# Performance work log

Measured on AMD Instinct MI355X. Metric: run time of the kernel, lower is better.

Reference implementation:

```python
import jax, jax.numpy as jnp
import numpy as np

# Tsit5 (Tsitouras 2011) explicit RK tableau coefficients (5th-order solution weights)
A21 = 0.161
A31, A32 = -0.008480655492356989, 0.335480655492357
A41, A42, A43 = 2.8971530571054935, -6.359448489975075, 4.3622954328695815
A51, A52, A53, A54 = 5.325864828439257, -11.748883564062828, 7.4955393428898365, -0.09249506636175525
A61, A62, A63, A64, A65 = 5.86145544294642, -12.92096931784711, 8.159367898576159, -0.071584973281401, -0.028269050394068383
B1, B2, B3, B4, B5, B6 = 0.09646076681806523, 0.01, 0.4798896504144996, 1.379008574103742, -3.290069515436081, 2.324710524099774

BATCH, D, H, T = 4096, 64, 256, 128


def net_apply(y, W1, b1, W2, b2):
    # y: [B, D] -> dy/dt: [B, D]  (MLP vector field, autonomous)
    return jnp.tanh(y @ W1 + b1) @ W2 + b2


def tsit5_step(f, y, h):
    # One explicit Tsit5 step of size h on state y: [B, D]
    k1 = f(y)
    k2 = f(y + h * (A21 * k1))
    k3 = f(y + h * (A31 * k1 + A32 * k2))
    k4 = f(y + h * (A41 * k1 + A42 * k2 + A43 * k3))
    k5 = f(y + h * (A51 * k1 + A52 * k2 + A53 * k3 + A54 * k4))
    k6 = f(y + h * (A61 * k1 + A62 * k2 + A63 * k3 + A64 * k4 + A65 * k5))
    return y + h * (B1 * k1 + B2 * k2 + B3 * k3 + B4 * k4 + B5 * k5 + B6 * k6)


def setup_inputs() -> dict:
    key = jax.random.key(0)
    k0, k1, k2 = jax.random.split(key, 3)
    y0 = jax.random.normal(k0, (BATCH, D), dtype=jnp.float32)
    ts = jnp.arange(T, dtype=jnp.float32) * 0.05  # save times
    W1 = jax.random.normal(k1, (D, H), dtype=jnp.float32) / np.sqrt(D)
    b1 = jnp.zeros((H,), dtype=jnp.float32)
    W2 = jax.random.normal(k2, (H, D), dtype=jnp.float32) / np.sqrt(H)
    b2 = jnp.zeros((D,), dtype=jnp.float32)
    return {"y0": y0, "ts": ts, "W1": W1, "b1": b1, "W2": W2, "b2": b2, "n_sub": 8}


def reference(y0, ts, W1, b1, W2, b2, n_sub):
    # Integrate dy/dt = net(y) with fixed-step Tsit5 (n_sub substeps per save interval),
    # returning the trajectory at save points ts: [B, T, D].
    f = lambda y: net_apply(y, W1, b1, W2, b2)

    def interval(y, dt):
        h = dt / n_sub
        def sub(yc, _):
            return tsit5_step(f, yc, h), None
        y, _ = jax.lax.scan(sub, y, None, length=n_sub)
        return y, y

    dts = jnp.diff(ts)                      # [T-1]
    _, ys = jax.lax.scan(interval, y0, dts)  # [T-1, B, D]
    traj = jnp.concatenate([y0[None], ys], axis=0)  # [T, B, D]
    return jnp.transpose(traj, (1, 0, 2))   # [B, T, D]
```

## Files before the change

### kernel.cpp

```cpp
#include <hip/hip_runtime.h>
#include <hip/hip_bf16.h>

typedef __bf16 bf16x8 __attribute__((ext_vector_type(8)));
typedef float f32x4 __attribute__((ext_vector_type(4)));

#define MFMA_B16(a,b,c) __builtin_amdgcn_mfma_f32_16x16x32_bf16((a),(b),(c),0,0,0)

#define A21f 0.161f
#define A31f (-0.008480655492356989f)
#define A32f 0.335480655492357f
#define A41f 2.8971530571054935f
#define A42f (-6.359448489975075f)
#define A43f 4.3622954328695815f
#define A51f 5.325864828439257f
#define A52f (-11.748883564062828f)
#define A53f 7.4955393428898365f
#define A54f (-0.09249506636175525f)
#define A61f 5.86145544294642f
#define A62f (-12.92096931784711f)
#define A63f 8.159367898576159f
#define A64f (-0.071584973281401f)
#define A65f (-0.028269050394068383f)
#define B1f 0.09646076681806523f
#define B2f 0.01f
#define B3f 0.4798896504144996f
#define B4f 1.379008574103742f
#define B5f (-3.290069515436081f)
#define B6f 2.324710524099774f

constexpr int T_SAVE = 128;
constexpr int DIM = 64;
constexpr int HID = 256;

__device__ __forceinline__ float fast_exp2(float x){
#if __has_builtin(__builtin_amdgcn_exp2f)
  return __builtin_amdgcn_exp2f(x);
#else
  return exp2f(x);
#endif
}
__device__ __forceinline__ float fast_rcp(float x){
#if __has_builtin(__builtin_amdgcn_rcpf)
  return __builtin_amdgcn_rcpf(x);
#else
  return 1.0f / x;
#endif
}
__device__ __forceinline__ float tanh_fast(float x){
  float t = fast_exp2(x * 2.8853900817779268f);
  return 1.0f - 2.0f * fast_rcp(t + 1.0f);
}

__global__ __launch_bounds__(512, 2)
void node_tsit5_kernel(const float* __restrict__ y0, const float* __restrict__ ts,
                       const float* __restrict__ W1g, const float* __restrict__ b1g,
                       const float* __restrict__ W2g, const float* __restrict__ b2g,
                       const int* __restrict__ nsub_p, float* __restrict__ out)
{
  const int tid = (int)threadIdx.x;
  const int w   = tid >> 6;
  const int l   = tid & 63;
  const int c   = l & 15;
  const int g   = l >> 4;
  const int wq  = w & 3;
  const int kh  = w >> 2;
  const bool hiW = (kh == 0);
  const int rowbase = (int)blockIdx.x * 16;

  __shared__ __align__(16) __bf16 Yh[2*64*8];
  __shared__ __align__(16) __bf16 Yl[2*64*8];
  __shared__ __align__(16) __bf16 Hh[8*64*8];
  __shared__ __align__(16) __bf16 Hl[8*64*8];
  __shared__ __align__(16) f32x4 Pex[8*64];
  __shared__ float ts_s[T_SAVE];

  if (tid < T_SAVE) ts_s[tid] = ts[tid];

  const int nsub = nsub_p[0];

  bf16x8 w1h[2][2], w1l[2][2], w2h[4], w2l[4];
#pragma unroll
  for (int nt = 0; nt < 2; ++nt) {
    const int col = (2*w + nt)*16 + c;
#pragma unroll
    for (int ks = 0; ks < 2; ++ks)
#pragma unroll
      for (int j = 0; j < 8; ++j) {
        float v = W1g[(ks*32 + g*8 + j)*HID + col];
        __bf16 hi = (__bf16)v;
        w1h[nt][ks][j] = hi;
        w1l[nt][ks][j] = (__bf16)(v - (float)hi);
      }
  }
#pragma unroll
  for (int i = 0; i < 4; ++i) {
    const int ks = 4*kh + i;
#pragma unroll
    for (int j = 0; j < 8; ++j) {
      float v = W2g[(ks*32 + g*8 + j)*DIM + (wq*16 + c)];
      __bf16 hi = (__bf16)v;
      w2h[i][j] = hi;
      w2l[i][j] = (__bf16)(v - (float)hi);
    }
  }
  float b1v[2];
#pragma unroll
  for (int nt = 0; nt < 2; ++nt) b1v[nt] = b1g[(2*w + nt)*16 + c];
  const float b2v = b2g[wq*16 + c];

  const int d_    = wq*16 + c;
  const int physL = l ^ ((l >> 3) & 3);

  int yoff[4];
#pragma unroll
  for (int s = 0; s < 4; ++s) {
    int row = 4*g + s;
    int lp  = row | (((d_ >> 3) & 3) << 4);
    int ph  = lp ^ ((lp >> 3) & 3);
    yoff[s] = (d_ >> 5)*512 + ph*8 + (d_ & 7);
  }
  int hoff[2][4];
#pragma unroll
  for (int nt = 0; nt < 2; ++nt) {
    int jcol = (2*w + nt)*16 + c;
#pragma unroll
    for (int r = 0; r < 4; ++r) {
      int row = 4*g + r;
      int lp  = row | (((jcol >> 3) & 3) << 4);
      int ph  = lp ^ ((lp >> 3) & 3);
      hoff[nt][r] = (jcol >> 5)*512 + ph*8 + (jcol & 7);
    }
  }

  float y[4];
#pragma unroll
  for (int s = 0; s < 4; ++s) {
    int row = rowbase + 4*g + s;
    y[s] = y0[row*DIM + d_];
    if (hiW) out[(size_t)row*(T_SAVE*DIM) + d_] = y[s];
  }
  __syncthreads();

  float k1[4], k2[4], k3[4], k4[4], k5[4], k6[4], ysv[4];
#pragma unroll
  for (int s = 0; s < 4; ++s) ysv[s] = y[s];

  auto feval = [&](float (&kout)[4]) {
#pragma unroll
    for (int s = 0; s < 4; ++s) {
      __bf16 hi = (__bf16)ysv[s];
      if (hiW) Yh[yoff[s]] = hi;
      else     Yl[yoff[s]] = (__bf16)(ysv[s] - (float)hi);
    }
    __syncthreads();
    bf16x8 ah0 = *(const bf16x8*)&Yh[physL*8];
    bf16x8 ah1 = *(const bf16x8*)&Yh[512 + physL*8];
    bf16x8 al0 = *(const bf16x8*)&Yl[physL*8];
    bf16x8 al1 = *(const bf16x8*)&Yl[512 + physL*8];
    f32x4 acc[2];
#pragma unroll
    for (int nt = 0; nt < 2; ++nt) acc[nt] = f32x4{0.f,0.f,0.f,0.f};
#pragma unroll
    for (int nt = 0; nt < 2; ++nt) acc[nt] = MFMA_B16(ah0, w1h[nt][0], acc[nt]);
#pragma unroll
    for (int nt = 0; nt < 2; ++nt) acc[nt] = MFMA_B16(ah1, w1h[nt][1], acc[nt]);
#pragma unroll
    for (int nt = 0; nt < 2; ++nt) acc[nt] = MFMA_B16(ah0, w1l[nt][0], acc[nt]);
#pragma unroll
    for (int nt = 0; nt < 2; ++nt) acc[nt] = MFMA_B16(ah1, w1l[nt][1], acc[nt]);
#pragma unroll
    for (int nt = 0; nt < 2; ++nt) acc[nt] = MFMA_B16(al0, w1h[nt][0], acc[nt]);
#pragma unroll
    for (int nt = 0; nt < 2; ++nt) acc[nt] = MFMA_B16(al1, w1h[nt][1], acc[nt]);
#pragma unroll
    for (int nt = 0; nt < 2; ++nt)
#pragma unroll
      for (int r = 0; r < 4; ++r) {
        float th = tanh_fast(acc[nt][r] + b1v[nt]);
        __bf16 hi = (__bf16)th;
        Hh[hoff[nt][r]] = hi;
        Hl[hoff[nt][r]] = (__bf16)(th - (float)hi);
      }
    __syncthreads();
    f32x4 a2[3];
#pragma unroll
    for (int i = 0; i < 3; ++i) a2[i] = f32x4{0.f,0.f,0.f,0.f};
#pragma unroll
    for (int i = 0; i < 4; ++i) {
      const int ks = 4*kh + i;
      bf16x8 ah = *(const bf16x8*)&Hh[ks*512 + physL*8];
      bf16x8 al = *(const bf16x8*)&Hl[ks*512 + physL*8];
      a2[0] = MFMA_B16(ah, w2h[i], a2[0]);
      a2[1] = MFMA_B16(ah, w2l[i], a2[1]);
      a2[2] = MFMA_B16(al, w2h[i], a2[2]);
    }
    f32x4 ps = (a2[0] + a2[1]) + a2[2];
    Pex[w*64 + l] = ps;
    __syncthreads();
    f32x4 qs = Pex[(w ^ 4)*64 + l];
#pragma unroll
    for (int s = 0; s < 4; ++s)
      kout[s] = (ps[s] + qs[s]) + b2v;
  };

  for (int iv = 0; iv < T_SAVE-1; ++iv) {
    const float h = (ts_s[iv+1] - ts_s[iv]) / (float)nsub;
    for (int sub = 0; sub < nsub; ++sub) {
      feval(k1);
#pragma unroll
      for (int s = 0; s < 4; ++s) ysv[s] = fmaf(h, A21f*k1[s], y[s]);
      feval(k2);
#pragma unroll
      for (int s = 0; s < 4; ++s) {
        float t = fmaf(A32f, k2[s], A31f*k1[s]);
        ysv[s] = fmaf(h, t, y[s]);
      }
      feval(k3);
#pragma unroll
      for (int s = 0; s < 4; ++s) {
        float t = A41f*k1[s];
        t = fmaf(A42f, k2[s], t);
        t = fmaf(A43f, k3[s], t);
        ysv[s] = fmaf(h, t, y[s]);
      }
      feval(k4);
#pragma unroll
      for (int s = 0; s < 4; ++s) {
        float t = A51f*k1[s];
        t = fmaf(A52f, k2[s], t);
        t = fmaf(A53f, k3[s], t);
        t = fmaf(A54f, k4[s], t);
        ysv[s] = fmaf(h, t, y[s]);
      }
      feval(k5);
#pragma unroll
      for (int s = 0; s < 4; ++s) {
        float t = A61f*k1[s];
        t = fmaf(A62f, k2[s], t);
        t = fmaf(A63f, k3[s], t);
        t = fmaf(A64f, k4[s], t);
        t = fmaf(A65f, k5[s], t);
        ysv[s] = fmaf(h, t, y[s]);
      }
      feval(k6);
#pragma unroll
      for (int s = 0; s < 4; ++s) {
        float t = B1f*k1[s];
        t = fmaf(B2f, k2[s], t);
        t = fmaf(B3f, k3[s], t);
        t = fmaf(B4f, k4[s], t);
        t = fmaf(B5f, k5[s], t);
        t = fmaf(B6f, k6[s], t);
        y[s] = fmaf(h, t, y[s]);
        ysv[s] = y[s];
      }
    }
    if (hiW) {
#pragma unroll
      for (int s = 0; s < 4; ++s) {
        int row = rowbase + 4*g + s;
        out[(size_t)row*(T_SAVE*DIM) + (size_t)(iv+1)*DIM + d_] = y[s];
      }
    }
  }
}

extern "C" void kernel_launch(void* const* d_in, const int* in_sizes, int n_in,
                              void* d_out, int out_size, void* d_ws, size_t ws_size,
                              hipStream_t stream) {
  const float* y0 = (const float*)d_in[0];
  const float* ts = (const float*)d_in[1];
  const float* W1 = (const float*)d_in[2];
  const float* b1 = (const float*)d_in[3];
  const float* W2 = (const float*)d_in[4];
  const float* b2 = (const float*)d_in[5];
  const int* nsub = (const int*)d_in[6];
  float* out = (float*)d_out;

  const int Bnum = in_sizes[0] / DIM;
  const int nblocks = Bnum / 16;
  node_tsit5_kernel<<<nblocks, 512, 0, stream>>>(y0, ts, W1, b1, W2, b2, nsub, out);
}
```

Measured before the change: 7.033 ms.

## Split per-block work across 16 waves with four-way K reduction

Doubles the block to 1024 threads (16 waves), so each wave computes one 16-column hidden tile and a quarter of the second-layer K range instead of two tiles and half. The partial sums of the second layer are reduced four ways through shared memory, and only the first 8 waves hold the RK state. This is meant to shorten the per-wave serial MFMA chain in each function evaluation by spreading it over more waves. In exchange it adds more threads waiting at every barrier, a larger reduction buffer, and 8 waves that sit idle during the RK stage updates.

```diff
diff --git a/kernel.cpp b/kernel.cpp
--- a/kernel.cpp
+++ b/kernel.cpp
@@ -51,7 +51,7 @@
   return 1.0f - 2.0f * fast_rcp(t + 1.0f);
 }
 
-__global__ __launch_bounds__(512, 2)
+__global__ __launch_bounds__(1024, 4)
 void node_tsit5_kernel(const float* __restrict__ y0, const float* __restrict__ ts,
                        const float* __restrict__ W1g, const float* __restrict__ b1g,
                        const float* __restrict__ W2g, const float* __restrict__ b2g,
@@ -63,38 +63,35 @@
   const int c   = l & 15;
   const int g   = l >> 4;
   const int wq  = w & 3;
-  const int kh  = w >> 2;
-  const bool hiW = (kh == 0);
+  const int kq  = w >> 2;
+  const bool stateW = (kq < 2);
+  const bool hiW    = (kq == 0);
   const int rowbase = (int)blockIdx.x * 16;
 
   __shared__ __align__(16) __bf16 Yh[2*64*8];
   __shared__ __align__(16) __bf16 Yl[2*64*8];
   __shared__ __align__(16) __bf16 Hh[8*64*8];
   __shared__ __align__(16) __bf16 Hl[8*64*8];
-  __shared__ __align__(16) f32x4 Pex[8*64];
+  __shared__ __align__(16) f32x4 Pex[16*64];
   __shared__ float ts_s[T_SAVE];
 
   if (tid < T_SAVE) ts_s[tid] = ts[tid];
 
   const int nsub = nsub_p[0];
 
-  bf16x8 w1h[2][2], w1l[2][2], w2h[4], w2l[4];
-#pragma unroll
-  for (int nt = 0; nt < 2; ++nt) {
-    const int col = (2*w + nt)*16 + c;
-#pragma unroll
-    for (int ks = 0; ks < 2; ++ks)
-#pragma unroll
-      for (int j = 0; j < 8; ++j) {
-        float v = W1g[(ks*32 + g*8 + j)*HID + col];
-        __bf16 hi = (__bf16)v;
-        w1h[nt][ks][j] = hi;
-        w1l[nt][ks][j] = (__bf16)(v - (float)hi);
-      }
-  }
-#pragma unroll
-  for (int i = 0; i < 4; ++i) {
-    const int ks = 4*kh + i;
+  bf16x8 w1h[2], w1l[2], w2h[2], w2l[2];
+#pragma unroll
+  for (int ks = 0; ks < 2; ++ks)
+#pragma unroll
+    for (int j = 0; j < 8; ++j) {
+      float v = W1g[(ks*32 + g*8 + j)*HID + (w*16 + c)];
+      __bf16 hi = (__bf16)v;
+      w1h[ks][j] = hi;
+      w1l[ks][j] = (__bf16)(v - (float)hi);
+    }
+#pragma unroll
+  for (int i = 0; i < 2; ++i) {
+    const int ks = 2*kq + i;
 #pragma unroll
     for (int j = 0; j < 8; ++j) {
       float v = W2g[(ks*32 + g*8 + j)*DIM + (wq*16 + c)];
@@ -103,9 +100,7 @@
       w2l[i][j] = (__bf16)(v - (float)hi);
     }
   }
-  float b1v[2];
-#pragma unroll
-  for (int nt = 0; nt < 2; ++nt) b1v[nt] = b1g[(2*w + nt)*16 + c];
+  const float b1v = b1g[w*16 + c];
   const float b2v = b2g[wq*16 + c];
 
   const int d_    = wq*16 + c;
@@ -119,25 +114,26 @@
     int ph  = lp ^ ((lp >> 3) & 3);
     yoff[s] = (d_ >> 5)*512 + ph*8 + (d_ & 7);
   }
-  int hoff[2][4];
-#pragma unroll
-  for (int nt = 0; nt < 2; ++nt) {
-    int jcol = (2*w + nt)*16 + c;
+  int hoff[4];
+  {
+    int jcol = w*16 + c;
 #pragma unroll
     for (int r = 0; r < 4; ++r) {
       int row = 4*g + r;
       int lp  = row | (((jcol >> 3) & 3) << 4);
       int ph  = lp ^ ((lp >> 3) & 3);
-      hoff[nt][r] = (jcol >> 5)*512 + ph*8 + (jcol & 7);
-    }
-  }
-
-  float y[4];
-#pragma unroll
-  for (int s = 0; s < 4; ++s) {
-    int row = rowbase + 4*g + s;
-    y[s] = y0[row*DIM + d_];
-    if (hiW) out[(size_t)row*(T_SAVE*DIM) + d_] = y[s];
+      hoff[r] = (jcol >> 5)*512 + ph*8 + (jcol & 7);
+    }
+  }
+
+  float y[4] = {0.f,0.f,0.f,0.f};
+  if (stateW) {
+#pragma unroll
+    for (int s = 0; s < 4; ++s) {
+      int row = rowbase + 4*g + s;
+      y[s] = y0[row*DIM + d_];
+      if (hiW) out[(size_t)row*(T_SAVE*DIM) + d_] = y[s];
+    }
   }
   __syncthreads();
 
@@ -146,113 +142,120 @@
   for (int s = 0; s < 4; ++s) ysv[s] = y[s];
 
   auto feval = [&](float (&kout)[4]) {
-#pragma unroll
-    for (int s = 0; s < 4; ++s) {
-      __bf16 hi = (__bf16)ysv[s];
-      if (hiW) Yh[yoff[s]] = hi;
-      else     Yl[yoff[s]] = (__bf16)(ysv[s] - (float)hi);
+    if (stateW) {
+#pragma unroll
+      for (int s = 0; s < 4; ++s) {
+        __bf16 hi = (__bf16)ysv[s];
+        if (hiW) Yh[yoff[s]] = hi;
+        else     Yl[yoff[s]] = (__bf16)(ysv[s] - (float)hi);
+      }
     }
     __syncthreads();
     bf16x8 ah0 = *(const bf16x8*)&Yh[physL*8];
     bf16x8 ah1 = *(const bf16x8*)&Yh[512 + physL*8];
     bf16x8 al0 = *(const bf16x8*)&Yl[physL*8];
     bf16x8 al1 = *(const bf16x8*)&Yl[512 + physL*8];
-    f32x4 acc[2];
-#pragma unroll
-    for (int nt = 0; nt < 2; ++nt) acc[nt] = f32x4{0.f,0.f,0.f,0.f};
-#pragma unroll
-    for (int nt = 0; nt < 2; ++nt) acc[nt] = MFMA_B16(ah0, w1h[nt][0], acc[nt]);
-#pragma unroll
-    for (int nt = 0; nt < 2; ++nt) acc[nt] = MFMA_B16(ah1, w1h[nt][1], acc[nt]);
-#pragma unroll
-    for (int nt = 0; nt < 2; ++nt) acc[nt] = MFMA_B16(ah0, w1l[nt][0], acc[nt]);
-#pragma unroll
-    for (int nt = 0; nt < 2; ++nt) acc[nt] = MFMA_B16(ah1, w1l[nt][1], acc[nt]);
-#pragma unroll
-    for (int nt = 0; nt < 2; ++nt) acc[nt] = MFMA_B16(al0, w1h[nt][0], acc[nt]);
-#pragma unroll
-    for (int nt = 0; nt < 2; ++nt) acc[nt] = MFMA_B16(al1, w1h[nt][1], acc[nt]);
-#pragma unroll
-    for (int nt = 0; nt < 2; ++nt)
-#pragma unroll
-      for (int r = 0; r < 4; ++r) {
-        float th = tanh_fast(acc[nt][r] + b1v[nt]);
-        __bf16 hi = (__bf16)th;
-        Hh[hoff[nt][r]] = hi;
-        Hl[hoff[nt][r]] = (__bf16)(th - (float)hi);
-      }
+    f32x4 acc0 = {0.f,0.f,0.f,0.f}, acc1 = {0.f,0.f,0.f,0.f};
+    acc0 = MFMA_B16(ah0, w1h[0], acc0);
+    acc1 = MFMA_B16(ah1, w1h[1], acc1);
+    acc0 = MFMA_B16(ah0, w1l[0], acc0);
+    acc1 = MFMA_B16(ah1, w1l[1], acc1);
+    acc0 = MFMA_B16(al0, w1h[0], acc0);
+    acc1 = MFMA_B16(al1, w1h[1], acc1);
+    f32x4 hsum = acc0 + acc1;
+#pragma unroll
+    for (int r = 0; r < 4; ++r) {
+      float th = tanh_fast(hsum[r] + b1v);
+      __bf16 hi = (__bf16)th;
+      Hh[hoff[r]] = hi;
+      Hl[hoff[r]] = (__bf16)(th - (float)hi);
+    }
     __syncthreads();
-    f32x4 a2[3];
-#pragma unroll
-    for (int i = 0; i < 3; ++i) a2[i] = f32x4{0.f,0.f,0.f,0.f};
-#pragma unroll
-    for (int i = 0; i < 4; ++i) {
-      const int ks = 4*kh + i;
+    f32x4 aA = {0.f,0.f,0.f,0.f}, aB = {0.f,0.f,0.f,0.f};
+#pragma unroll
+    for (int i = 0; i < 2; ++i) {
+      const int ks = 2*kq + i;
       bf16x8 ah = *(const bf16x8*)&Hh[ks*512 + physL*8];
       bf16x8 al = *(const bf16x8*)&Hl[ks*512 + physL*8];
-      a2[0] = MFMA_B16(ah, w2h[i], a2[0]);
-      a2[1] = MFMA_B16(ah, w2l[i], a2[1]);
-      a2[2] = MFMA_B16(al, w2h[i], a2[2]);
-    }
-    f32x4 ps = (a2[0] + a2[1]) + a2[2];
-    Pex[w*64 + l] = ps;
+      aA = MFMA_B16(ah, w2h[i], aA);
+      aB = MFMA_B16(ah, w2l[i], aB);
+      aB = MFMA_B16(al, w2h[i], aB);
+    }
+    Pex[w*64 + l] = aA + aB;
     __syncthreads();
-    f32x4 qs = Pex[(w ^ 4)*64 + l];
-#pragma unroll
-    for (int s = 0; s < 4; ++s)
-      kout[s] = (ps[s] + qs[s]) + b2v;
+    if (stateW) {
+      f32x4 q0 = Pex[(wq     )*64 + l];
+      f32x4 q1 = Pex[(wq +  4)*64 + l];
+      f32x4 q2 = Pex[(wq +  8)*64 + l];
+      f32x4 q3 = Pex[(wq + 12)*64 + l];
+      f32x4 kk = (q0 + q1) + (q2 + q3);
+#pragma unroll
+      for (int s = 0; s < 4; ++s) kout[s] = kk[s] + b2v;
+    }
   };
 
   for (int iv = 0; iv < T_SAVE-1; ++iv) {
     const float h = (ts_s[iv+1] - ts_s[iv]) / (float)nsub;
     for (int sub = 0; sub < nsub; ++sub) {
       feval(k1);
-#pragma unroll
-      for (int s = 0; s < 4; ++s) ysv[s] = fmaf(h, A21f*k1[s], y[s]);
+      if (stateW) {
+#pragma unroll
+        for (int s = 0; s < 4; ++s) ysv[s] = fmaf(h, A21f*k1[s], y[s]);
+      }
       feval(k2);
-#pragma unroll
-      for (int s = 0; s < 4; ++s) {
-        float t = fmaf(A32f, k2[s], A31f*k1[s]);
-        ysv[s] = fmaf(h, t, y[s]);
+      if (stateW) {
+#pragma unroll
+        for (int s = 0; s < 4; ++s) {
+          float t = fmaf(A32f, k2[s], A31f*k1[s]);
+          ysv[s] = fmaf(h, t, y[s]);
+        }
       }
       feval(k3);
-#pragma unroll
-      for (int s = 0; s < 4; ++s) {
-        float t = A41f*k1[s];
-        t = fmaf(A42f, k2[s], t);
-        t = fmaf(A43f, k3[s], t);
-        ysv[s] = fmaf(h, t, y[s]);
+      if (stateW) {
+#pragma unroll
+        for (int s = 0; s < 4; ++s) {
+          float t = A41f*k1[s];
+          t = fmaf(A42f, k2[s], t);
+          t = fmaf(A43f, k3[s], t);
+          ysv[s] = fmaf(h, t, y[s]);
+        }
       }
       feval(k4);
-#pragma unroll
-      for (int s = 0; s < 4; ++s) {
-        float t = A51f*k1[s];
-        t = fmaf(A52f, k2[s], t);
-        t = fmaf(A53f, k3[s], t);
-        t = fmaf(A54f, k4[s], t);
-        ysv[s] = fmaf(h, t, y[s]);
+      if (stateW) {
+#pragma unroll
+        for (int s = 0; s < 4; ++s) {
+          float t = A51f*k1[s];
+          t = fmaf(A52f, k2[s], t);
+          t = fmaf(A53f, k3[s], t);
+          t = fmaf(A54f, k4[s], t);
+          ysv[s] = fmaf(h, t, y[s]);
+        }
       }
       feval(k5);
-#pragma unroll
-      for (int s = 0; s < 4; ++s) {
-        float t = A61f*k1[s];
-        t = fmaf(A62f, k2[s], t);
-        t = fmaf(A63f, k3[s], t);
-        t = fmaf(A64f, k4[s], t);
-        t = fmaf(A65f, k5[s], t);
-        ysv[s] = fmaf(h, t, y[s]);
+      if (stateW) {
+#pragma unroll
+        for (int s = 0; s < 4; ++s) {
+          float t = A61f*k1[s];
+          t = fmaf(A62f, k2[s], t);
+          t = fmaf(A63f, k3[s], t);
+          t = fmaf(A64f, k4[s], t);
+          t = fmaf(A65f, k5[s], t);
+          ysv[s] = fmaf(h, t, y[s]);
+        }
       }
       feval(k6);
-#pragma unroll
-      for (int s = 0; s < 4; ++s) {
-        float t = B1f*k1[s];
-        t = fmaf(B2f, k2[s], t);
-        t = fmaf(B3f, k3[s], t);
-        t = fmaf(B4f, k4[s], t);
-        t = fmaf(B5f, k5[s], t);
-        t = fmaf(B6f, k6[s], t);
-        y[s] = fmaf(h, t, y[s]);
-        ysv[s] = y[s];
+      if (stateW) {
+#pragma unroll
+        for (int s = 0; s < 4; ++s) {
+          float t = B1f*k1[s];
+          t = fmaf(B2f, k2[s], t);
+          t = fmaf(B3f, k3[s], t);
+          t = fmaf(B4f, k4[s], t);
+          t = fmaf(B5f, k5[s], t);
+          t = fmaf(B6f, k6[s], t);
+          y[s] = fmaf(h, t, y[s]);
+          ysv[s] = y[s];
+        }
       }
     }
     if (hiW) {
@@ -279,5 +282,5 @@
 
   const int Bnum = in_sizes[0] / DIM;
   const int nblocks = Bnum / 16;
-  node_tsit5_kernel<<<nblocks, 512, 0, stream>>>(y0, ts, W1, b1, W2, b2, nsub, out);
-}
+  node_tsit5_kernel<<<nblocks, 1024, 0, stream>>>(y0, ts, W1, b1, W2, b2, nsub, out);
+}
```

New measurement: 7.325 ms. 4.1% more time.

## Drop cross-wave partial-sum exchange by giving each wave the full W2 K-range

Applied to the files above, without the earlier changes.

Each wave now holds all eight K-slices of W2 in registers and computes the full second-layer product, so the shared-memory partial-sum exchange and its extra barrier per function evaluation are removed. The first-layer MFMAs are split into two independent accumulator chains to shorten dependency stalls, and the RK stage combinations are expressed as 4-wide vector arithmetic. The trade-off is that every wave does twice the second-layer MFMA work, pairs of waves compute the same output redundantly, and register pressure rises, which may hurt occupancy under the 512x2 launch bound.

```diff
diff --git a/kernel.cpp b/kernel.cpp
--- a/kernel.cpp
+++ b/kernel.cpp
@@ -50,6 +50,7 @@
   float t = fast_exp2(x * 2.8853900817779268f);
   return 1.0f - 2.0f * fast_rcp(t + 1.0f);
 }
+__device__ __forceinline__ f32x4 splat4(float x){ return f32x4{x,x,x,x}; }
 
 __global__ __launch_bounds__(512, 2)
 void node_tsit5_kernel(const float* __restrict__ y0, const float* __restrict__ ts,
@@ -63,22 +64,20 @@
   const int c   = l & 15;
   const int g   = l >> 4;
   const int wq  = w & 3;
-  const int kh  = w >> 2;
-  const bool hiW = (kh == 0);
+  const bool hiW = (w < 4);
   const int rowbase = (int)blockIdx.x * 16;
 
   __shared__ __align__(16) __bf16 Yh[2*64*8];
   __shared__ __align__(16) __bf16 Yl[2*64*8];
   __shared__ __align__(16) __bf16 Hh[8*64*8];
   __shared__ __align__(16) __bf16 Hl[8*64*8];
-  __shared__ __align__(16) f32x4 Pex[8*64];
   __shared__ float ts_s[T_SAVE];
 
   if (tid < T_SAVE) ts_s[tid] = ts[tid];
 
   const int nsub = nsub_p[0];
 
-  bf16x8 w1h[2][2], w1l[2][2], w2h[4], w2l[4];
+  bf16x8 w1h[2][2], w1l[2][2];
 #pragma unroll
   for (int nt = 0; nt < 2; ++nt) {
     const int col = (2*w + nt)*16 + c;
@@ -92,17 +91,16 @@
         w1l[nt][ks][j] = (__bf16)(v - (float)hi);
       }
   }
-#pragma unroll
-  for (int i = 0; i < 4; ++i) {
-    const int ks = 4*kh + i;
+  bf16x8 w2h[8], w2l[8];
+#pragma unroll
+  for (int ks = 0; ks < 8; ++ks)
 #pragma unroll
     for (int j = 0; j < 8; ++j) {
       float v = W2g[(ks*32 + g*8 + j)*DIM + (wq*16 + c)];
       __bf16 hi = (__bf16)v;
-      w2h[i][j] = hi;
-      w2l[i][j] = (__bf16)(v - (float)hi);
-    }
-  }
+      w2h[ks][j] = hi;
+      w2l[ks][j] = (__bf16)(v - (float)hi);
+    }
   float b1v[2];
 #pragma unroll
   for (int nt = 0; nt < 2; ++nt) b1v[nt] = b1g[(2*w + nt)*16 + c];
@@ -132,134 +130,110 @@
     }
   }
 
-  float y[4];
+  f32x4 y4;
 #pragma unroll
   for (int s = 0; s < 4; ++s) {
     int row = rowbase + 4*g + s;
-    y[s] = y0[row*DIM + d_];
-    if (hiW) out[(size_t)row*(T_SAVE*DIM) + d_] = y[s];
+    y4[s] = y0[row*DIM + d_];
+    if (hiW) out[(size_t)row*(T_SAVE*DIM) + d_] = y4[s];
   }
   __syncthreads();
 
-  float k1[4], k2[4], k3[4], k4[4], k5[4], k6[4], ysv[4];
-#pragma unroll
-  for (int s = 0; s < 4; ++s) ysv[s] = y[s];
-
-  auto feval = [&](float (&kout)[4]) {
-#pragma unroll
-    for (int s = 0; s < 4; ++s) {
-      __bf16 hi = (__bf16)ysv[s];
-      if (hiW) Yh[yoff[s]] = hi;
-      else     Yl[yoff[s]] = (__bf16)(ysv[s] - (float)hi);
+  f32x4 ysv = y4;
+
+  auto feval = [&]() -> f32x4 {
+    if (hiW) {
+#pragma unroll
+      for (int s = 0; s < 4; ++s) Yh[yoff[s]] = (__bf16)ysv[s];
+    } else {
+#pragma unroll
+      for (int s = 0; s < 4; ++s) {
+        float hi = (float)(__bf16)ysv[s];
+        Yl[yoff[s]] = (__bf16)(ysv[s] - hi);
+      }
     }
     __syncthreads();
     bf16x8 ah0 = *(const bf16x8*)&Yh[physL*8];
     bf16x8 ah1 = *(const bf16x8*)&Yh[512 + physL*8];
     bf16x8 al0 = *(const bf16x8*)&Yl[physL*8];
     bf16x8 al1 = *(const bf16x8*)&Yl[512 + physL*8];
-    f32x4 acc[2];
-#pragma unroll
-    for (int nt = 0; nt < 2; ++nt) acc[nt] = f32x4{0.f,0.f,0.f,0.f};
-#pragma unroll
-    for (int nt = 0; nt < 2; ++nt) acc[nt] = MFMA_B16(ah0, w1h[nt][0], acc[nt]);
-#pragma unroll
-    for (int nt = 0; nt < 2; ++nt) acc[nt] = MFMA_B16(ah1, w1h[nt][1], acc[nt]);
-#pragma unroll
-    for (int nt = 0; nt < 2; ++nt) acc[nt] = MFMA_B16(ah0, w1l[nt][0], acc[nt]);
-#pragma unroll
-    for (int nt = 0; nt < 2; ++nt) acc[nt] = MFMA_B16(ah1, w1l[nt][1], acc[nt]);
-#pragma unroll
-    for (int nt = 0; nt < 2; ++nt) acc[nt] = MFMA_B16(al0, w1h[nt][0], acc[nt]);
-#pragma unroll
-    for (int nt = 0; nt < 2; ++nt) acc[nt] = MFMA_B16(al1, w1h[nt][1], acc[nt]);
-#pragma unroll
-    for (int nt = 0; nt < 2; ++nt)
-#pragma unroll
-      for (int r = 0; r < 4; ++r) {
-        float th = tanh_fast(acc[nt][r] + b1v[nt]);
-        __bf16 hi = (__bf16)th;
-        Hh[hoff[nt][r]] = hi;
-        Hl[hoff[nt][r]] = (__bf16)(th - (float)hi);
-      }
+    f32x4 p0 = {0.f,0.f,0.f,0.f}, q0 = {0.f,0.f,0.f,0.f};
+    f32x4 p1 = {0.f,0.f,0.f,0.f}, q1 = {0.f,0.f,0.f,0.f};
+    p0 = MFMA_B16(ah0, w1h[0][0], p0);  q0 = MFMA_B16(ah1, w1h[0][1], q0);
+    p1 = MFMA_B16(ah0, w1h[1][0], p1);  q1 = MFMA_B16(ah1, w1h[1][1], q1);
+    p0 = MFMA_B16(ah0, w1l[0][0], p0);  q0 = MFMA_B16(ah1, w1l[0][1], q0);
+    p1 = MFMA_B16(ah0, w1l[1][0], p1);  q1 = MFMA_B16(ah1, w1l[1][1], q1);
+    p0 = MFMA_B16(al0, w1h[0][0], p0);  q0 = MFMA_B16(al1, w1h[0][1], q0);
+    p1 = MFMA_B16(al0, w1h[1][0], p1);  q1 = MFMA_B16(al1, w1h[1][1], q1);
+    f32x4 h0 = p0 + q0, h1 = p1 + q1;
+#pragma unroll
+    for (int r = 0; r < 4; ++r) {
+      float th = tanh_fast(h0[r] + b1v[0]);
+      __bf16 hi = (__bf16)th;
+      Hh[hoff[0][r]] = hi;
+      Hl[hoff[0][r]] = (__bf16)(th - (float)hi);
+    }
+#pragma unroll
+    for (int r = 0; r < 4; ++r) {
+      float th = tanh_fast(h1[r] + b1v[1]);
+      __bf16 hi = (__bf16)th;
+      Hh[hoff[1][r]] = hi;
+      Hl[hoff[1][r]] = (__bf16)(th - (float)hi);
+    }
     __syncthreads();
-    f32x4 a2[3];
-#pragma unroll
-    for (int i = 0; i < 3; ++i) a2[i] = f32x4{0.f,0.f,0.f,0.f};
-#pragma unroll
-    for (int i = 0; i < 4; ++i) {
-      const int ks = 4*kh + i;
+    f32x4 aA = {0.f,0.f,0.f,0.f}, aB = {0.f,0.f,0.f,0.f}, aC = {0.f,0.f,0.f,0.f};
+#pragma unroll
+    for (int ks = 0; ks < 8; ++ks) {
       bf16x8 ah = *(const bf16x8*)&Hh[ks*512 + physL*8];
       bf16x8 al = *(const bf16x8*)&Hl[ks*512 + physL*8];
-      a2[0] = MFMA_B16(ah, w2h[i], a2[0]);
-      a2[1] = MFMA_B16(ah, w2l[i], a2[1]);
-      a2[2] = MFMA_B16(al, w2h[i], a2[2]);
-    }
-    f32x4 ps = (a2[0] + a2[1]) + a2[2];
-    Pex[w*64 + l] = ps;
-    __syncthreads();
-    f32x4 qs = Pex[(w ^ 4)*64 + l];
-#pragma unroll
-    for (int s = 0; s < 4; ++s)
-      kout[s] = (ps[s] + qs[s]) + b2v;
+      aA = MFMA_B16(ah, w2h[ks], aA);
+      aB = MFMA_B16(ah, w2l[ks], aB);
+      aC = MFMA_B16(al, w2h[ks], aC);
+    }
+    return (aA + aB) + aC + splat4(b2v);
   };
 
   for (int iv = 0; iv < T_SAVE-1; ++iv) {
     const float h = (ts_s[iv+1] - ts_s[iv]) / (float)nsub;
+    const f32x4 h4 = splat4(h);
     for (int sub = 0; sub < nsub; ++sub) {
-      feval(k1);
-#pragma unroll
-      for (int s = 0; s < 4; ++s) ysv[s] = fmaf(h, A21f*k1[s], y[s]);
-      feval(k2);
-#pragma unroll
-      for (int s = 0; s < 4; ++s) {
-        float t = fmaf(A32f, k2[s], A31f*k1[s]);
-        ysv[s] = fmaf(h, t, y[s]);
-      }
-      feval(k3);
-#pragma unroll
-      for (int s = 0; s < 4; ++s) {
-        float t = A41f*k1[s];
-        t = fmaf(A42f, k2[s], t);
-        t = fmaf(A43f, k3[s], t);
-        ysv[s] = fmaf(h, t, y[s]);
-      }
-      feval(k4);
-#pragma unroll
-      for (int s = 0; s < 4; ++s) {
-        float t = A51f*k1[s];
-        t = fmaf(A52f, k2[s], t);
-        t = fmaf(A53f, k3[s], t);
-        t = fmaf(A54f, k4[s], t);
-        ysv[s] = fmaf(h, t, y[s]);
-      }
-      feval(k5);
-#pragma unroll
-      for (int s = 0; s < 4; ++s) {
-        float t = A61f*k1[s];
-        t = fmaf(A62f, k2[s], t);
-        t = fmaf(A63f, k3[s], t);
-        t = fmaf(A64f, k4[s], t);
-        t = fmaf(A65f, k5[s], t);
-        ysv[s] = fmaf(h, t, y[s]);
-      }
-      feval(k6);
-#pragma unroll
-      for (int s = 0; s < 4; ++s) {
-        float t = B1f*k1[s];
-        t = fmaf(B2f, k2[s], t);
-        t = fmaf(B3f, k3[s], t);
-        t = fmaf(B4f, k4[s], t);
-        t = fmaf(B5f, k5[s], t);
-        t = fmaf(B6f, k6[s], t);
-        y[s] = fmaf(h, t, y[s]);
-        ysv[s] = y[s];
+      f32x4 k1 = feval();
+      ysv = y4 + h4 * (splat4(A21f) * k1);
+      f32x4 k2 = feval();
+      {
+        f32x4 t = splat4(A31f)*k1 + splat4(A32f)*k2;
+        ysv = y4 + h4 * t;
+      }
+      f32x4 k3 = feval();
+      {
+        f32x4 t = splat4(A41f)*k1 + splat4(A42f)*k2 + splat4(A43f)*k3;
+        ysv = y4 + h4 * t;
+      }
+      f32x4 k4 = feval();
+      {
+        f32x4 t = splat4(A51f)*k1 + splat4(A52f)*k2 + splat4(A53f)*k3
+                + splat4(A54f)*k4;
+        ysv = y4 + h4 * t;
+      }
+      f32x4 k5 = feval();
+      {
+        f32x4 t = splat4(A61f)*k1 + splat4(A62f)*k2 + splat4(A63f)*k3
+                + splat4(A64f)*k4 + splat4(A65f)*k5;
+        ysv = y4 + h4 * t;
+      }
+      f32x4 k6 = feval();
+      {
+        f32x4 t = splat4(B1f)*k1 + splat4(B2f)*k2 + splat4(B3f)*k3
+                + splat4(B4f)*k4 + splat4(B5f)*k5 + splat4(B6f)*k6;
+        y4 = y4 + h4 * t;
+        ysv = y4;
       }
     }
     if (hiW) {
 #pragma unroll
       for (int s = 0; s < 4; ++s) {
         int row = rowbase + 4*g + s;
-        out[(size_t)row*(T_SAVE*DIM) + (size_t)(iv+1)*DIM + d_] = y[s];
+        out[(size_t)row*(T_SAVE*DIM) + (size_t)(iv+1)*DIM + d_] = y4[s];
       }
     }
   }
```

After: 7.351 ms. +4.5%, slower.
